# Kernel optimization log

Measured on AMD Instinct MI355X. Metric: run time of the kernel, lower is better.

Reference implementation:

```python
import jax, jax.numpy as jnp
import numpy as np

XZ = jnp.array([0, 2])
XY = jnp.array([0, 1])
YZ = jnp.array([1, 2])


def _bilinear(plane, uv):
    """plane: (C,R,R) as (C,H,W); uv: (N,2) in [0,1], uv[:,0]->width, uv[:,1]->height.
    Border padding + align_corners=True semantics (grid_sample style)."""
    R = plane.shape[-1]
    xy = jnp.clip(uv, 0.0, 1.0) * (R - 1)
    x, y = xy[:, 0], xy[:, 1]
    x0 = jnp.floor(x)
    y0 = jnp.floor(y)
    x0i = jnp.clip(x0.astype(jnp.int32), 0, R - 1)
    y0i = jnp.clip(y0.astype(jnp.int32), 0, R - 1)
    x1i = jnp.clip(x0i + 1, 0, R - 1)
    y1i = jnp.clip(y0i + 1, 0, R - 1)
    wx = (x - x0)[None, :]  # (1,N)
    wy = (y - y0)[None, :]
    f00 = plane[:, y0i, x0i]  # (C,N)
    f01 = plane[:, y0i, x1i]
    f10 = plane[:, y1i, x0i]
    f11 = plane[:, y1i, x1i]
    top = f00 * (1.0 - wx) + f01 * wx
    bot = f10 * (1.0 - wx) + f11 * wx
    return (top * (1.0 - wy) + bot * wy).T  # (N,C)


def _sample_triplane(p, c_xz, c_xy, c_yz):
    """p: (bs,N,3) in [0,1]; planes: (bs,C,R,R). Returns (bs,N,C) summed over planes."""
    def per_batch(pb, fxz, fxy, fyz):
        return (_bilinear(fxz, pb[:, XZ])
                + _bilinear(fxy, pb[:, XY])
                + _bilinear(fyz, pb[:, YZ]))
    return jax.vmap(per_batch)(p, c_xz, c_xy, c_yz)


def setup_inputs() -> dict:
    key = jax.random.key(0)
    ks = jax.random.split(key, 12)
    bs, ns, C, S, R = 2, 50000, 32, 8, 128
    inp = {
        "query_pos": jax.random.uniform(ks[0], (bs, ns, 3), dtype=jnp.float32),
        "c_xz": jax.random.normal(ks[1], (bs, C, R, R), dtype=jnp.float32),
        "c_xy": jax.random.normal(ks[2], (bs, C, R, R), dtype=jnp.float32),
        "c_yz": jax.random.normal(ks[3], (bs, C, R, R), dtype=jnp.float32),
        # offset weights scaled small so sampled points stay mostly in-bounds
        "W_off": jax.random.normal(ks[4], (C, S * 3), dtype=jnp.float32) * 0.01,
        "b_off": jnp.zeros((S * 3,), dtype=jnp.float32),
        "W_w": jax.random.normal(ks[5], (C, S), dtype=jnp.float32) * 0.1,
        "b_w": jnp.zeros((S,), dtype=jnp.float32),
        "W_v": jax.random.normal(ks[6], (C, C), dtype=jnp.float32) * (1.0 / np.sqrt(C)),
        "b_v": jnp.zeros((C,), dtype=jnp.float32),
        "W_out": jax.random.normal(ks[7], (C, C), dtype=jnp.float32) * (1.0 / np.sqrt(C)),
        "b_out": jnp.zeros((C,), dtype=jnp.float32),
    }
    return inp


def reference(query_pos, c_xz, c_xy, c_yz, W_off, b_off, W_w, b_w, W_v, b_v, W_out, b_out):
    bs, ns, _ = query_pos.shape
    S = W_w.shape[1]
    # round 1: sample tri-plane features at query points
    feature = _sample_triplane(query_pos, c_xz, c_xy, c_yz)  # (bs,ns,C)
    # predict per-query sample offsets and weights
    off = (feature @ W_off + b_off).reshape(bs, ns, S, 3)
    w = (feature @ W_w + b_w).reshape(bs, ns, S, 1)
    pts = off + query_pos[:, :, None, :]  # (bs,ns,S,3)
    # round 2: sample at deformed points
    aux = _sample_triplane(pts.reshape(bs, ns * S, 3), c_xz, c_xy, c_yz)
    v = aux.reshape(bs, ns, S, -1) @ W_v + b_v  # (bs,ns,S,C)
    out = (v * w).sum(-2)                        # weighted reduce over samples
    out = out @ W_out + b_out + feature          # residual
    return out  # (bs,ns,C)
```

## Files before the change

kernel.cpp:

```cpp
#include <hip/hip_runtime.h>
#include <hip/hip_fp16.h>

#define BS 2
#define NS 50000
#define CCH 32
#define RR 128
#define SS 8

typedef float v2f __attribute__((ext_vector_type(2)));


__device__ __forceinline__ v2f unpk(unsigned u) {
    __half2 h = __builtin_bit_cast(__half2, u);
    float2 f = __half22float2(h);
    v2f r; r.x = f.x; r.y = f.y;
    return r;
}

__global__ __launch_bounds__(256)
void prep(const float* __restrict__ cxz,
          const float* __restrict__ cxy,
          const float* __restrict__ cyz,
          const float* __restrict__ Wv, const float* __restrict__ bv,
          const float* __restrict__ Wout,
          unsigned short* __restrict__ tp, float* __restrict__ Wc,
          float* __restrict__ bvw) {
    __shared__ float lds[32 * 129];
    int tid = threadIdx.x;
    int row = blockIdx.x;
    if (row < BS * 3 * RR) {
        int y  = row & 127;
        int pl = (row >> 7) % 3;
        int b  = row / 384;
        const float* src = (pl == 0) ? cxz : ((pl == 1) ? cxy : cyz);
        const float* sp = src + (((size_t)(b * CCH)) << 14) + (y << 7);
#pragma unroll
        for (int i = 0; i < 16; ++i) {
            int c = (tid >> 7) + 2 * i;
            int x = tid & 127;
            lds[c * 129 + x] = sp[((size_t)c << 14) + x];
        }
        __syncthreads();
        ushort2* dst = (ushort2*)(tp + ((size_t)row << 12));
#pragma unroll
        for (int i = 0; i < 8; ++i) {
            int c2 = tid & 15;
            int x  = (tid >> 4) + 16 * i;
            ushort2 v;
            v.x = __half_as_ushort(__float2half(lds[(2 * c2) * 129 + x]));
            v.y = __half_as_ushort(__float2half(lds[(2 * c2 + 1) * 129 + x]));
            dst[(x << 4) + c2] = v;
        }
    } else {
        int t = (row - BS * 3 * RR) * 256 + tid;
        int c = t >> 5, j = t & 31;
        float acc = 0.f;
#pragma unroll
        for (int k = 0; k < 32; ++k) acc += Wv[c * 32 + k] * Wout[k * 32 + j];
        Wc[t] = acc;
        if (t < 32) {
            float a2 = 0.f;
#pragma unroll
            for (int k = 0; k < 32; ++k) a2 += bv[k] * Wout[k * 32 + t];
            bvw[t] = a2;
        }
    }
}

struct f4v { v2f lo, hi; };

__device__ __forceinline__ f4v sample3_h(const uint2* __restrict__ P0,
                                         float p0, float p1, float p2) {
    float ux[3] = {p0, p0, p1};
    float uy[3] = {p2, p1, p2};
    v2f rlo = {0.f, 0.f}, rhi = {0.f, 0.f};
#pragma unroll
    for (int pl = 0; pl < 3; ++pl) {
        float x = fminf(fmaxf(ux[pl], 0.f), 1.f) * 127.f;
        float y = fminf(fmaxf(uy[pl], 0.f), 1.f) * 127.f;
        float x0f = floorf(x), y0f = floorf(y);
        int x0 = (int)x0f, y0 = (int)y0f;
        int x1 = min(x0 + 1, 127), y1 = min(y0 + 1, 127);
        float wx = x - x0f, wy = y - y0f;
        const uint2* P = P0 + ((size_t)pl << 17);
        int r0 = (y0 << 10), r1 = (y1 << 10);
        uint2 u00 = P[r0 + (x0 << 3)];
        uint2 u01 = P[r0 + (x1 << 3)];
        uint2 u10 = P[r1 + (x0 << 3)];
        uint2 u11 = P[r1 + (x1 << 3)];
        v2f wx2 = {wx, wx}, wy2 = {wy, wy};
        {
            v2f f00 = unpk(u00.x), f01 = unpk(u01.x);
            v2f t = __builtin_elementwise_fma(wx2, f01 - f00, f00);
            v2f f10 = unpk(u10.x), f11 = unpk(u11.x);
            v2f bo = __builtin_elementwise_fma(wx2, f11 - f10, f10);
            rlo += __builtin_elementwise_fma(wy2, bo - t, t);
        }
        {
            v2f f00 = unpk(u00.y), f01 = unpk(u01.y);
            v2f t = __builtin_elementwise_fma(wx2, f01 - f00, f00);
            v2f f10 = unpk(u10.y), f11 = unpk(u11.y);
            v2f bo = __builtin_elementwise_fma(wx2, f11 - f10, f10);
            rhi += __builtin_elementwise_fma(wy2, bo - t, t);
        }
    }
    f4v r; r.lo = rlo; r.hi = rhi; return r;
}

#define GETE(v, idx) (((idx) & 2) ? (((idx) & 1) ? (v).hi.y : (v).hi.x) \
                                  : (((idx) & 1) ? (v).lo.y : (v).lo.x))
#define GETC(v, idx) __shfl(GETE(v, idx), base | ((idx) >> 2), 64)

__global__ __launch_bounds__(256)
void eda_main(const float* __restrict__ qp, const unsigned short* __restrict__ tp,
              const float* __restrict__ Woff, const float* __restrict__ boff,
              const float* __restrict__ Ww, const float* __restrict__ bw,
              const float* __restrict__ Wc, const float* __restrict__ bvw,
              const float* __restrict__ bout, float* __restrict__ out) {
    __shared__ v2f sWcat[32][8][2];
    __shared__ v2f sWc[32][8][2];
    __shared__ float sbcat[32];
    __shared__ float sbvw[32];
    __shared__ float sbout[32];

    int tid = threadIdx.x;
    for (int i = tid; i < 1024; i += 256) {
        int k = i >> 5, j = i & 31;
        ((float*)sWcat)[i] = (j < 24) ? Woff[k * 24 + j] : Ww[k * 8 + (j - 24)];
        ((float*)sWc)[i]   = Wc[i];
    }
    if (tid < 32) {
        sbcat[tid] = (tid < 24) ? boff[tid] : bw[tid - 24];
        sbvw[tid]  = bvw[tid];
        sbout[tid] = bout[tid];
    }
    __syncthreads();

    int lane = tid & 7;
    int base = tid & 56;
    int b  = blockIdx.x & 1;
    int qi = (blockIdx.x >> 1) * 32 + (tid >> 3);
    int qq = min(qi, NS - 1);

    const float* p = qp + ((size_t)b * NS + qq) * 3;
    float p0 = p[0], p1 = p[1], p2 = p[2];

    const uint2* P0 = (const uint2*)tp + (((size_t)(b * 3)) << 17) + lane;

    f4v feat = sample3_h(P0, p0, p1, p2);

    f4v cat;
    cat.lo.x = sbcat[(lane << 2) + 0]; cat.lo.y = sbcat[(lane << 2) + 1];
    cat.hi.x = sbcat[(lane << 2) + 2]; cat.hi.y = sbcat[(lane << 2) + 3];
#pragma unroll
    for (int k = 0; k < 32; ++k) {
        float fc = GETC(feat, k);
        v2f fc2 = {fc, fc};
        cat.lo = __builtin_elementwise_fma(fc2, sWcat[k][lane][0], cat.lo);
        cat.hi = __builtin_elementwise_fma(fc2, sWcat[k][lane][1], cat.hi);
    }

    float w_s[SS], o0[SS], o1[SS], o2[SS];
#pragma unroll
    for (int s = 0; s < SS; ++s) {
        w_s[s] = GETC(cat, 24 + s);
        o0[s]  = GETC(cat, 3 * s + 0);
        o1[s]  = GETC(cat, 3 * s + 1);
        o2[s]  = GETC(cat, 3 * s + 2);
    }

    f4v wa; wa.lo = (v2f){0.f, 0.f}; wa.hi = (v2f){0.f, 0.f};
    float wsum = 0.f;
#pragma unroll
    for (int s = 0; s < SS; ++s) {
        f4v aux = sample3_h(P0, p0 + o0[s], p1 + o1[s], p2 + o2[s]);
        v2f w2 = {w_s[s], w_s[s]};
        wa.lo = __builtin_elementwise_fma(w2, aux.lo, wa.lo);
        wa.hi = __builtin_elementwise_fma(w2, aux.hi, wa.hi);
        wsum += w_s[s];
    }

    v2f ws2 = {wsum, wsum};
    v2f blo = {sbout[(lane << 2) + 0], sbout[(lane << 2) + 1]};
    v2f bhi = {sbout[(lane << 2) + 2], sbout[(lane << 2) + 3]};
    v2f vlo = {sbvw[(lane << 2) + 0], sbvw[(lane << 2) + 1]};
    v2f vhi = {sbvw[(lane << 2) + 2], sbvw[(lane << 2) + 3]};
    v2f olo = __builtin_elementwise_fma(ws2, vlo, blo) + feat.lo;
    v2f ohi = __builtin_elementwise_fma(ws2, vhi, bhi) + feat.hi;
#pragma unroll
    for (int k = 0; k < 32; ++k) {
        float wc = GETC(wa, k);
        v2f wc2 = {wc, wc};
        olo = __builtin_elementwise_fma(wc2, sWc[k][lane][0], olo);
        ohi = __builtin_elementwise_fma(wc2, sWc[k][lane][1], ohi);
    }

    if (qi < NS) {
        float4 o4 = make_float4(olo.x, olo.y, ohi.x, ohi.y);
        *(float4*)(out + ((size_t)b * NS + qi) * 32 + (lane << 2)) = o4;
    }
}

extern "C" void kernel_launch(void* const* d_in, const int* in_sizes, int n_in,
                              void* d_out, int out_size, void* d_ws, size_t ws_size,
                              hipStream_t stream) {
    const float* qp   = (const float*)d_in[0];
    const float* cxz  = (const float*)d_in[1];
    const float* cxy  = (const float*)d_in[2];
    const float* cyz  = (const float*)d_in[3];
    const float* Woff = (const float*)d_in[4];
    const float* boff = (const float*)d_in[5];
    const float* Ww   = (const float*)d_in[6];
    const float* bw   = (const float*)d_in[7];
    const float* Wv   = (const float*)d_in[8];
    const float* bv   = (const float*)d_in[9];
    const float* Wout = (const float*)d_in[10];
    const float* bout = (const float*)d_in[11];
    float* out = (float*)d_out;

    unsigned short* tp = (unsigned short*)d_ws;
    float* Wc  = (float*)((char*)d_ws + (size_t)BS * 3 * RR * RR * CCH * 2);
    float* bvw = Wc + 1024;

    prep<<<BS * 3 * RR + 4, 256, 0, stream>>>(cxz, cxy, cyz, Wv, bv, Wout, tp, Wc, bvw);
    eda_main<<<2 * ((NS + 31) / 32), 256, 0, stream>>>(qp, tp, Woff, boff, Ww, bw,
                                                       Wc, bvw, bout, out);
}
```

Before: 141.5 us.

## Batch tap loads for two samples before evaluating, shrink blocks to 128 threads

Restructures trilinear sampling so all 12 gather loads for a sample are issued first, and two deformed samples' taps are loaded together before any arithmetic, increasing memory-level parallelism. Bilinear weights are precomputed as four corner weights, so each tap becomes a direct FMA. Block size drops to 128 threads with 16 queries per block, and the tail bounds checks are removed because NS divides evenly by 16. More live loads raise register pressure, which may reduce occupancy.

```diff
diff --git a/kernel.cpp b/kernel.cpp
--- a/kernel.cpp
+++ b/kernel.cpp
@@ -9,13 +9,6 @@
 
 typedef float v2f __attribute__((ext_vector_type(2)));
 
-
-__device__ __forceinline__ v2f unpk(unsigned u) {
-    __half2 h = __builtin_bit_cast(__half2, u);
-    float2 f = __half22float2(h);
-    v2f r; r.x = f.x; r.y = f.y;
-    return r;
-}
 
 __global__ __launch_bounds__(256)
 void prep(const float* __restrict__ cxz,
@@ -67,51 +60,60 @@
     }
 }
 
+
+struct Taps { uint2 u[12]; float wgt[12]; };
+
+__device__ __forceinline__ void load_plane(const uint2* __restrict__ P,
+                                           float px, float py,
+                                           uint2* u, float* wgt) {
+    float x = fminf(fmaxf(px, 0.f), 1.f) * 127.f;
+    float y = fminf(fmaxf(py, 0.f), 1.f) * 127.f;
+    float x0f = floorf(x), y0f = floorf(y);
+    int x0 = (int)x0f, y0 = (int)y0f;
+    int x1 = min(x0 + 1, 127), y1 = min(y0 + 1, 127);
+    float wx = x - x0f, wy = y - y0f;
+    int r0 = (y0 << 10), r1 = (y1 << 10);
+    u[0] = P[r0 + (x0 << 3)];
+    u[1] = P[r0 + (x1 << 3)];
+    u[2] = P[r1 + (x0 << 3)];
+    u[3] = P[r1 + (x1 << 3)];
+    float w11 = wx * wy;
+    wgt[1] = wx - w11;
+    wgt[2] = wy - w11;
+    wgt[0] = 1.f - wx - wgt[2];
+    wgt[3] = w11;
+}
+
+__device__ __forceinline__ Taps load_taps(const uint2* __restrict__ P0,
+                                          float p0, float p1, float p2) {
+    Taps t;
+    load_plane(P0,                      p0, p2, t.u + 0, t.wgt + 0);
+    load_plane(P0 + ((size_t)1 << 17),  p0, p1, t.u + 4, t.wgt + 4);
+    load_plane(P0 + ((size_t)2 << 17),  p1, p2, t.u + 8, t.wgt + 8);
+    return t;
+}
+
+__device__ __forceinline__ void acc4(v2f& lo, v2f& hi, uint2 u, float w) {
+    __half2 a = __builtin_bit_cast(__half2, u.x);
+    __half2 b = __builtin_bit_cast(__half2, u.y);
+    lo.x = fmaf(__half2float(a.x), w, lo.x);
+    lo.y = fmaf(__half2float(a.y), w, lo.y);
+    hi.x = fmaf(__half2float(b.x), w, hi.x);
+    hi.y = fmaf(__half2float(b.y), w, hi.y);
+}
+
+__device__ __forceinline__ void eval_taps(const Taps& t, v2f& lo, v2f& hi) {
+#pragma unroll
+    for (int i = 0; i < 12; ++i) acc4(lo, hi, t.u[i], t.wgt[i]);
+}
+
 struct f4v { v2f lo, hi; };
-
-__device__ __forceinline__ f4v sample3_h(const uint2* __restrict__ P0,
-                                         float p0, float p1, float p2) {
-    float ux[3] = {p0, p0, p1};
-    float uy[3] = {p2, p1, p2};
-    v2f rlo = {0.f, 0.f}, rhi = {0.f, 0.f};
-#pragma unroll
-    for (int pl = 0; pl < 3; ++pl) {
-        float x = fminf(fmaxf(ux[pl], 0.f), 1.f) * 127.f;
-        float y = fminf(fmaxf(uy[pl], 0.f), 1.f) * 127.f;
-        float x0f = floorf(x), y0f = floorf(y);
-        int x0 = (int)x0f, y0 = (int)y0f;
-        int x1 = min(x0 + 1, 127), y1 = min(y0 + 1, 127);
-        float wx = x - x0f, wy = y - y0f;
-        const uint2* P = P0 + ((size_t)pl << 17);
-        int r0 = (y0 << 10), r1 = (y1 << 10);
-        uint2 u00 = P[r0 + (x0 << 3)];
-        uint2 u01 = P[r0 + (x1 << 3)];
-        uint2 u10 = P[r1 + (x0 << 3)];
-        uint2 u11 = P[r1 + (x1 << 3)];
-        v2f wx2 = {wx, wx}, wy2 = {wy, wy};
-        {
-            v2f f00 = unpk(u00.x), f01 = unpk(u01.x);
-            v2f t = __builtin_elementwise_fma(wx2, f01 - f00, f00);
-            v2f f10 = unpk(u10.x), f11 = unpk(u11.x);
-            v2f bo = __builtin_elementwise_fma(wx2, f11 - f10, f10);
-            rlo += __builtin_elementwise_fma(wy2, bo - t, t);
-        }
-        {
-            v2f f00 = unpk(u00.y), f01 = unpk(u01.y);
-            v2f t = __builtin_elementwise_fma(wx2, f01 - f00, f00);
-            v2f f10 = unpk(u10.y), f11 = unpk(u11.y);
-            v2f bo = __builtin_elementwise_fma(wx2, f11 - f10, f10);
-            rhi += __builtin_elementwise_fma(wy2, bo - t, t);
-        }
-    }
-    f4v r; r.lo = rlo; r.hi = rhi; return r;
-}
 
 #define GETE(v, idx) (((idx) & 2) ? (((idx) & 1) ? (v).hi.y : (v).hi.x) \
                                   : (((idx) & 1) ? (v).lo.y : (v).lo.x))
 #define GETC(v, idx) __shfl(GETE(v, idx), base | ((idx) >> 2), 64)
 
-__global__ __launch_bounds__(256)
+__global__ __launch_bounds__(128)
 void eda_main(const float* __restrict__ qp, const unsigned short* __restrict__ tp,
               const float* __restrict__ Woff, const float* __restrict__ boff,
               const float* __restrict__ Ww, const float* __restrict__ bw,
@@ -124,7 +126,7 @@
     __shared__ float sbout[32];
 
     int tid = threadIdx.x;
-    for (int i = tid; i < 1024; i += 256) {
+    for (int i = tid; i < 1024; i += 128) {
         int k = i >> 5, j = i & 31;
         ((float*)sWcat)[i] = (j < 24) ? Woff[k * 24 + j] : Ww[k * 8 + (j - 24)];
         ((float*)sWc)[i]   = Wc[i];
@@ -139,15 +141,18 @@
     int lane = tid & 7;
     int base = tid & 56;
     int b  = blockIdx.x & 1;
-    int qi = (blockIdx.x >> 1) * 32 + (tid >> 3);
-    int qq = min(qi, NS - 1);
-
-    const float* p = qp + ((size_t)b * NS + qq) * 3;
+    int qi = (blockIdx.x >> 1) * 16 + (tid >> 3);
+
+    const float* p = qp + ((size_t)b * NS + qi) * 3;
     float p0 = p[0], p1 = p[1], p2 = p[2];
 
     const uint2* P0 = (const uint2*)tp + (((size_t)(b * 3)) << 17) + lane;
 
-    f4v feat = sample3_h(P0, p0, p1, p2);
+    f4v feat; feat.lo = (v2f){0.f, 0.f}; feat.hi = (v2f){0.f, 0.f};
+    {
+        Taps t = load_taps(P0, p0, p1, p2);
+        eval_taps(t, feat.lo, feat.hi);
+    }
 
     f4v cat;
     cat.lo.x = sbcat[(lane << 2) + 0]; cat.lo.y = sbcat[(lane << 2) + 1];
@@ -172,12 +177,20 @@
     f4v wa; wa.lo = (v2f){0.f, 0.f}; wa.hi = (v2f){0.f, 0.f};
     float wsum = 0.f;
 #pragma unroll
-    for (int s = 0; s < SS; ++s) {
-        f4v aux = sample3_h(P0, p0 + o0[s], p1 + o1[s], p2 + o2[s]);
-        v2f w2 = {w_s[s], w_s[s]};
-        wa.lo = __builtin_elementwise_fma(w2, aux.lo, wa.lo);
-        wa.hi = __builtin_elementwise_fma(w2, aux.hi, wa.hi);
-        wsum += w_s[s];
+    for (int s = 0; s < SS; s += 2) {
+        Taps t0 = load_taps(P0, p0 + o0[s],     p1 + o1[s],     p2 + o2[s]);
+        Taps t1 = load_taps(P0, p0 + o0[s + 1], p1 + o1[s + 1], p2 + o2[s + 1]);
+        f4v a0; a0.lo = (v2f){0.f, 0.f}; a0.hi = (v2f){0.f, 0.f};
+        f4v a1; a1.lo = (v2f){0.f, 0.f}; a1.hi = (v2f){0.f, 0.f};
+        eval_taps(t0, a0.lo, a0.hi);
+        eval_taps(t1, a1.lo, a1.hi);
+        v2f w20 = {w_s[s], w_s[s]};
+        v2f w21 = {w_s[s + 1], w_s[s + 1]};
+        wa.lo = __builtin_elementwise_fma(w20, a0.lo, wa.lo);
+        wa.hi = __builtin_elementwise_fma(w20, a0.hi, wa.hi);
+        wa.lo = __builtin_elementwise_fma(w21, a1.lo, wa.lo);
+        wa.hi = __builtin_elementwise_fma(w21, a1.hi, wa.hi);
+        wsum += w_s[s] + w_s[s + 1];
     }
 
     v2f ws2 = {wsum, wsum};
@@ -195,10 +208,8 @@
         ohi = __builtin_elementwise_fma(wc2, sWc[k][lane][1], ohi);
     }
 
-    if (qi < NS) {
-        float4 o4 = make_float4(olo.x, olo.y, ohi.x, ohi.y);
-        *(float4*)(out + ((size_t)b * NS + qi) * 32 + (lane << 2)) = o4;
-    }
+    float4 o4 = make_float4(olo.x, olo.y, ohi.x, ohi.y);
+    *(float4*)(out + ((size_t)b * NS + qi) * 32 + (lane << 2)) = o4;
 }
 
 extern "C" void kernel_launch(void* const* d_in, const int* in_sizes, int n_in,
@@ -223,6 +234,6 @@
     float* bvw = Wc + 1024;
 
     prep<<<BS * 3 * RR + 4, 256, 0, stream>>>(cxz, cxy, cyz, Wv, bv, Wout, tp, Wc, bvw);
-    eda_main<<<2 * ((NS + 31) / 32), 256, 0, stream>>>(qp, tp, Woff, boff, Ww, bw,
-                                                       Wc, bvw, bout, out);
-}
+    eda_main<<<2 * (NS / 16), 128, 0, stream>>>(qp, tp, Woff, boff, Ww, bw,
+                                                Wc, bvw, bout, out);
+}
```

After: 140.2 us. About the same (-0.9%).

## Use 4 lanes per query with 16-byte gathers and weight-form bilinear

Applied to the files above, without the earlier changes.

Each query is now handled by 4 lanes instead of 8, and each lane loads 8 fp16 channels as one uint4 rather than 4 channels as a uint2. Block size drops to 128 threads while still covering 32 queries per block. Bilinear interpolation is rewritten as four corner weights accumulated with scalar FMAs, replacing the lerp form. The aim is to halve the number of gather instructions and the redundant coordinate math per query. The cost is more registers per lane and fewer threads to hide gather latency.

```diff
diff --git a/kernel.cpp b/kernel.cpp
--- a/kernel.cpp
+++ b/kernel.cpp
@@ -9,13 +9,6 @@
 
 typedef float v2f __attribute__((ext_vector_type(2)));
 
-
-__device__ __forceinline__ v2f unpk(unsigned u) {
-    __half2 h = __builtin_bit_cast(__half2, u);
-    float2 f = __half22float2(h);
-    v2f r; r.x = f.x; r.y = f.y;
-    return r;
-}
 
 __global__ __launch_bounds__(256)
 void prep(const float* __restrict__ cxz,
@@ -67,64 +60,80 @@
     }
 }
 
-struct f4v { v2f lo, hi; };
-
-__device__ __forceinline__ f4v sample3_h(const uint2* __restrict__ P0,
-                                         float p0, float p1, float p2) {
-    float ux[3] = {p0, p0, p1};
-    float uy[3] = {p2, p1, p2};
-    v2f rlo = {0.f, 0.f}, rhi = {0.f, 0.f};
-#pragma unroll
-    for (int pl = 0; pl < 3; ++pl) {
-        float x = fminf(fmaxf(ux[pl], 0.f), 1.f) * 127.f;
-        float y = fminf(fmaxf(uy[pl], 0.f), 1.f) * 127.f;
-        float x0f = floorf(x), y0f = floorf(y);
-        int x0 = (int)x0f, y0 = (int)y0f;
-        int x1 = min(x0 + 1, 127), y1 = min(y0 + 1, 127);
-        float wx = x - x0f, wy = y - y0f;
-        const uint2* P = P0 + ((size_t)pl << 17);
-        int r0 = (y0 << 10), r1 = (y1 << 10);
-        uint2 u00 = P[r0 + (x0 << 3)];
-        uint2 u01 = P[r0 + (x1 << 3)];
-        uint2 u10 = P[r1 + (x0 << 3)];
-        uint2 u11 = P[r1 + (x1 << 3)];
-        v2f wx2 = {wx, wx}, wy2 = {wy, wy};
-        {
-            v2f f00 = unpk(u00.x), f01 = unpk(u01.x);
-            v2f t = __builtin_elementwise_fma(wx2, f01 - f00, f00);
-            v2f f10 = unpk(u10.x), f11 = unpk(u11.x);
-            v2f bo = __builtin_elementwise_fma(wx2, f11 - f10, f10);
-            rlo += __builtin_elementwise_fma(wy2, bo - t, t);
-        }
-        {
-            v2f f00 = unpk(u00.y), f01 = unpk(u01.y);
-            v2f t = __builtin_elementwise_fma(wx2, f01 - f00, f00);
-            v2f f10 = unpk(u10.y), f11 = unpk(u11.y);
-            v2f bo = __builtin_elementwise_fma(wx2, f11 - f10, f10);
-            rhi += __builtin_elementwise_fma(wy2, bo - t, t);
-        }
-    }
-    f4v r; r.lo = rlo; r.hi = rhi; return r;
-}
-
-#define GETE(v, idx) (((idx) & 2) ? (((idx) & 1) ? (v).hi.y : (v).hi.x) \
-                                  : (((idx) & 1) ? (v).lo.y : (v).lo.x))
-#define GETC(v, idx) __shfl(GETE(v, idx), base | ((idx) >> 2), 64)
-
-__global__ __launch_bounds__(256)
+
+struct f8 { v2f a[4]; };
+
+__device__ __forceinline__ void acc8(f8& acc, uint4 u, float w) {
+    __half2 h0 = __builtin_bit_cast(__half2, u.x);
+    __half2 h1 = __builtin_bit_cast(__half2, u.y);
+    __half2 h2 = __builtin_bit_cast(__half2, u.z);
+    __half2 h3 = __builtin_bit_cast(__half2, u.w);
+    acc.a[0].x = fmaf(__half2float(h0.x), w, acc.a[0].x);
+    acc.a[0].y = fmaf(__half2float(h0.y), w, acc.a[0].y);
+    acc.a[1].x = fmaf(__half2float(h1.x), w, acc.a[1].x);
+    acc.a[1].y = fmaf(__half2float(h1.y), w, acc.a[1].y);
+    acc.a[2].x = fmaf(__half2float(h2.x), w, acc.a[2].x);
+    acc.a[2].y = fmaf(__half2float(h2.y), w, acc.a[2].y);
+    acc.a[3].x = fmaf(__half2float(h3.x), w, acc.a[3].x);
+    acc.a[3].y = fmaf(__half2float(h3.y), w, acc.a[3].y);
+}
+
+__device__ __forceinline__ void axq(float p, int& i0, int& i1, float& w) {
+    float x = fminf(fmaxf(p, 0.f), 1.f) * 127.f;
+    float f = floorf(x);
+    i0 = (int)f;
+    i1 = min(i0 + 1, 127);
+    w = x - f;
+}
+
+__device__ __forceinline__ void plane_acc(f8& acc, const uint4* __restrict__ P,
+                                          int xi0, int xi1, float wx,
+                                          int yi0, int yi1, float wy) {
+    int r0 = yi0 << 9, r1 = yi1 << 9;
+    int c0 = xi0 << 2, c1 = xi1 << 2;
+    uint4 u00 = P[r0 + c0];
+    uint4 u01 = P[r0 + c1];
+    uint4 u10 = P[r1 + c0];
+    uint4 u11 = P[r1 + c1];
+    float w11 = wx * wy;
+    float w01 = wx - w11;
+    float w10 = wy - w11;
+    float w00 = 1.f - wx - w10;
+    acc8(acc, u00, w00);
+    acc8(acc, u01, w01);
+    acc8(acc, u10, w10);
+    acc8(acc, u11, w11);
+}
+
+__device__ __forceinline__ void sample3(f8& acc, const uint4* __restrict__ P0,
+                                        float p0, float p1, float p2) {
+    int a0i0, a0i1, a1i0, a1i1, a2i0, a2i1;
+    float w0, w1, w2;
+    axq(p0, a0i0, a0i1, w0);
+    axq(p1, a1i0, a1i1, w1);
+    axq(p2, a2i0, a2i1, w2);
+    plane_acc(acc, P0,             a0i0, a0i1, w0, a2i0, a2i1, w2);
+    plane_acc(acc, P0 + (1 << 16), a0i0, a0i1, w0, a1i0, a1i1, w1);
+    plane_acc(acc, P0 + (2 << 16), a1i0, a1i1, w1, a2i0, a2i1, w2);
+}
+
+#define GETE(v, idx) (((idx) & 1) ? (v).a[((idx) >> 1) & 3].y : (v).a[((idx) >> 1) & 3].x)
+#define GETC(v, idx) __shfl(GETE(v, idx), base | ((idx) >> 3), 64)
+
+__global__ __launch_bounds__(128)
 void eda_main(const float* __restrict__ qp, const unsigned short* __restrict__ tp,
               const float* __restrict__ Woff, const float* __restrict__ boff,
               const float* __restrict__ Ww, const float* __restrict__ bw,
               const float* __restrict__ Wc, const float* __restrict__ bvw,
               const float* __restrict__ bout, float* __restrict__ out) {
-    __shared__ v2f sWcat[32][8][2];
-    __shared__ v2f sWc[32][8][2];
+    __shared__ v2f sWcat[32][4][4];
+    __shared__ v2f sWc[32][4][4];
     __shared__ float sbcat[32];
     __shared__ float sbvw[32];
     __shared__ float sbout[32];
 
     int tid = threadIdx.x;
-    for (int i = tid; i < 1024; i += 256) {
+    for (int i = tid; i < 1024; i += 128) {
         int k = i >> 5, j = i & 31;
         ((float*)sWcat)[i] = (j < 24) ? Woff[k * 24 + j] : Ww[k * 8 + (j - 24)];
         ((float*)sWc)[i]   = Wc[i];
@@ -136,28 +145,33 @@
     }
     __syncthreads();
 
-    int lane = tid & 7;
-    int base = tid & 56;
+    int lane = tid & 3;
+    int base = tid & 60;
     int b  = blockIdx.x & 1;
-    int qi = (blockIdx.x >> 1) * 32 + (tid >> 3);
+    int qi = (blockIdx.x >> 1) * 32 + (tid >> 2);
     int qq = min(qi, NS - 1);
 
     const float* p = qp + ((size_t)b * NS + qq) * 3;
     float p0 = p[0], p1 = p[1], p2 = p[2];
 
-    const uint2* P0 = (const uint2*)tp + (((size_t)(b * 3)) << 17) + lane;
-
-    f4v feat = sample3_h(P0, p0, p1, p2);
-
-    f4v cat;
-    cat.lo.x = sbcat[(lane << 2) + 0]; cat.lo.y = sbcat[(lane << 2) + 1];
-    cat.hi.x = sbcat[(lane << 2) + 2]; cat.hi.y = sbcat[(lane << 2) + 3];
+    const uint4* P0 = (const uint4*)tp + (((size_t)(b * 3)) << 16) + lane;
+
+    f8 feat = {};
+    sample3(feat, P0, p0, p1, p2);
+
+    f8 cat;
+#pragma unroll
+    for (int e = 0; e < 4; ++e) {
+        cat.a[e].x = sbcat[(lane << 3) + 2 * e];
+        cat.a[e].y = sbcat[(lane << 3) + 2 * e + 1];
+    }
 #pragma unroll
     for (int k = 0; k < 32; ++k) {
         float fc = GETC(feat, k);
         v2f fc2 = {fc, fc};
-        cat.lo = __builtin_elementwise_fma(fc2, sWcat[k][lane][0], cat.lo);
-        cat.hi = __builtin_elementwise_fma(fc2, sWcat[k][lane][1], cat.hi);
+#pragma unroll
+        for (int e = 0; e < 4; ++e)
+            cat.a[e] = __builtin_elementwise_fma(fc2, sWcat[k][lane][e], cat.a[e]);
     }
 
     float w_s[SS], o0[SS], o1[SS], o2[SS];
@@ -169,35 +183,40 @@
         o2[s]  = GETC(cat, 3 * s + 2);
     }
 
-    f4v wa; wa.lo = (v2f){0.f, 0.f}; wa.hi = (v2f){0.f, 0.f};
+    f8 wa = {};
     float wsum = 0.f;
 #pragma unroll
     for (int s = 0; s < SS; ++s) {
-        f4v aux = sample3_h(P0, p0 + o0[s], p1 + o1[s], p2 + o2[s]);
+        f8 aux = {};
+        sample3(aux, P0, p0 + o0[s], p1 + o1[s], p2 + o2[s]);
         v2f w2 = {w_s[s], w_s[s]};
-        wa.lo = __builtin_elementwise_fma(w2, aux.lo, wa.lo);
-        wa.hi = __builtin_elementwise_fma(w2, aux.hi, wa.hi);
+#pragma unroll
+        for (int e = 0; e < 4; ++e)
+            wa.a[e] = __builtin_elementwise_fma(w2, aux.a[e], wa.a[e]);
         wsum += w_s[s];
     }
 
+    f8 o;
     v2f ws2 = {wsum, wsum};
-    v2f blo = {sbout[(lane << 2) + 0], sbout[(lane << 2) + 1]};
-    v2f bhi = {sbout[(lane << 2) + 2], sbout[(lane << 2) + 3]};
-    v2f vlo = {sbvw[(lane << 2) + 0], sbvw[(lane << 2) + 1]};
-    v2f vhi = {sbvw[(lane << 2) + 2], sbvw[(lane << 2) + 3]};
-    v2f olo = __builtin_elementwise_fma(ws2, vlo, blo) + feat.lo;
-    v2f ohi = __builtin_elementwise_fma(ws2, vhi, bhi) + feat.hi;
+#pragma unroll
+    for (int e = 0; e < 4; ++e) {
+        v2f bo  = {sbout[(lane << 3) + 2 * e], sbout[(lane << 3) + 2 * e + 1]};
+        v2f bv2 = {sbvw[(lane << 3) + 2 * e], sbvw[(lane << 3) + 2 * e + 1]};
+        o.a[e] = __builtin_elementwise_fma(ws2, bv2, bo) + feat.a[e];
+    }
 #pragma unroll
     for (int k = 0; k < 32; ++k) {
         float wc = GETC(wa, k);
         v2f wc2 = {wc, wc};
-        olo = __builtin_elementwise_fma(wc2, sWc[k][lane][0], olo);
-        ohi = __builtin_elementwise_fma(wc2, sWc[k][lane][1], ohi);
+#pragma unroll
+        for (int e = 0; e < 4; ++e)
+            o.a[e] = __builtin_elementwise_fma(wc2, sWc[k][lane][e], o.a[e]);
     }
 
     if (qi < NS) {
-        float4 o4 = make_float4(olo.x, olo.y, ohi.x, ohi.y);
-        *(float4*)(out + ((size_t)b * NS + qi) * 32 + (lane << 2)) = o4;
+        float* dst = out + ((size_t)b * NS + qi) * 32 + (lane << 3);
+        *(float4*)dst       = make_float4(o.a[0].x, o.a[0].y, o.a[1].x, o.a[1].y);
+        *(float4*)(dst + 4) = make_float4(o.a[2].x, o.a[2].y, o.a[3].x, o.a[3].y);
     }
 }
 
@@ -223,6 +242,7 @@
     float* bvw = Wc + 1024;
 
     prep<<<BS * 3 * RR + 4, 256, 0, stream>>>(cxz, cxy, cyz, Wv, bv, Wout, tp, Wc, bvw);
-    eda_main<<<2 * ((NS + 31) / 32), 256, 0, stream>>>(qp, tp, Woff, boff, Ww, bw,
+    int blocks_per_batch = (NS + 31) / 32;
+    eda_main<<<2 * blocks_per_batch, 128, 0, stream>>>(qp, tp, Woff, boff, Ww, bw,
                                                        Wc, bvw, bout, out);
 }
```

Measured after the change: 138.3 us. 1.02x faster.

## Pack horizontal texel pairs in triplane layout and software-pipeline sample loads

Applied to the files above, without the earlier changes.

The prep kernel now stores each fp16 texel together with its x+1 neighbour in one 32-bit word, so a bilinear tap needs two 16-byte row loads per plane instead of four 8-byte loads. The main kernel splits sampling into a load phase and an evaluate phase and prefetches the next offset sample's loads while evaluating the current one. It also issues the first feature loads before staging the weights in LDS so their latency is hidden. In exchange the packed table is twice as large, raising prep write traffic and cache footprint, and holding a second sample's loads in flight raises register pressure.

```diff
diff --git a/kernel.cpp b/kernel.cpp
--- a/kernel.cpp
+++ b/kernel.cpp
@@ -9,13 +9,6 @@
 
 typedef float v2f __attribute__((ext_vector_type(2)));
 
-
-__device__ __forceinline__ v2f unpk(unsigned u) {
-    __half2 h = __builtin_bit_cast(__half2, u);
-    float2 f = __half22float2(h);
-    v2f r; r.x = f.x; r.y = f.y;
-    return r;
-}
 
 __global__ __launch_bounds__(256)
 void prep(const float* __restrict__ cxz,
@@ -23,7 +16,7 @@
           const float* __restrict__ cyz,
           const float* __restrict__ Wv, const float* __restrict__ bv,
           const float* __restrict__ Wout,
-          unsigned short* __restrict__ tp, float* __restrict__ Wc,
+          unsigned* __restrict__ tp, float* __restrict__ Wc,
           float* __restrict__ bvw) {
     __shared__ float lds[32 * 129];
     int tid = threadIdx.x;
@@ -41,15 +34,16 @@
             lds[c * 129 + x] = sp[((size_t)c << 14) + x];
         }
         __syncthreads();
-        ushort2* dst = (ushort2*)(tp + ((size_t)row << 12));
-#pragma unroll
-        for (int i = 0; i < 8; ++i) {
-            int c2 = tid & 15;
-            int x  = (tid >> 4) + 16 * i;
-            ushort2 v;
-            v.x = __half_as_ushort(__float2half(lds[(2 * c2) * 129 + x]));
-            v.y = __half_as_ushort(__float2half(lds[(2 * c2 + 1) * 129 + x]));
-            dst[(x << 4) + c2] = v;
+        unsigned* dst = tp + ((size_t)row << 12);
+#pragma unroll
+        for (int i = 0; i < 16; ++i) {
+            int idx = tid + 256 * i;
+            int c = idx & 31;
+            int x = idx >> 5;
+            int x1 = min(x + 1, 127);
+            unsigned h0 = __half_as_ushort(__float2half(lds[c * 129 + x]));
+            unsigned h1 = __half_as_ushort(__float2half(lds[c * 129 + x1]));
+            dst[(x << 5) + c] = h0 | (h1 << 16);
         }
     } else {
         int t = (row - BS * 3 * RR) * 256 + tid;
@@ -67,44 +61,65 @@
     }
 }
 
-struct f4v { v2f lo, hi; };
-
-__device__ __forceinline__ f4v sample3_h(const uint2* __restrict__ P0,
-                                         float p0, float p1, float p2) {
-    float ux[3] = {p0, p0, p1};
-    float uy[3] = {p2, p1, p2};
-    v2f rlo = {0.f, 0.f}, rhi = {0.f, 0.f};
-#pragma unroll
-    for (int pl = 0; pl < 3; ++pl) {
-        float x = fminf(fmaxf(ux[pl], 0.f), 1.f) * 127.f;
-        float y = fminf(fmaxf(uy[pl], 0.f), 1.f) * 127.f;
-        float x0f = floorf(x), y0f = floorf(y);
-        int x0 = (int)x0f, y0 = (int)y0f;
-        int x1 = min(x0 + 1, 127), y1 = min(y0 + 1, 127);
-        float wx = x - x0f, wy = y - y0f;
-        const uint2* P = P0 + ((size_t)pl << 17);
-        int r0 = (y0 << 10), r1 = (y1 << 10);
-        uint2 u00 = P[r0 + (x0 << 3)];
-        uint2 u01 = P[r0 + (x1 << 3)];
-        uint2 u10 = P[r1 + (x0 << 3)];
-        uint2 u11 = P[r1 + (x1 << 3)];
-        v2f wx2 = {wx, wx}, wy2 = {wy, wy};
-        {
-            v2f f00 = unpk(u00.x), f01 = unpk(u01.x);
-            v2f t = __builtin_elementwise_fma(wx2, f01 - f00, f00);
-            v2f f10 = unpk(u10.x), f11 = unpk(u11.x);
-            v2f bo = __builtin_elementwise_fma(wx2, f11 - f10, f10);
-            rlo += __builtin_elementwise_fma(wy2, bo - t, t);
-        }
-        {
-            v2f f00 = unpk(u00.y), f01 = unpk(u01.y);
-            v2f t = __builtin_elementwise_fma(wx2, f01 - f00, f00);
-            v2f f10 = unpk(u10.y), f11 = unpk(u11.y);
-            v2f bo = __builtin_elementwise_fma(wx2, f11 - f10, f10);
-            rhi += __builtin_elementwise_fma(wy2, bo - t, t);
-        }
-    }
-    f4v r; r.lo = rlo; r.hi = rhi; return r;
+
+struct f4 { v2f lo, hi; };
+
+struct Samp { uint4 u[6]; float wc0, wc1, wr1, wr2; };
+
+__device__ __forceinline__ Samp load_samp(const uint4* __restrict__ P0,
+                                          float p0, float p1, float p2) {
+    Samp t;
+    float x0c = fminf(fmaxf(p0, 0.f), 1.f) * 127.f;
+    float x1c = fminf(fmaxf(p1, 0.f), 1.f) * 127.f;
+    float x2c = fminf(fmaxf(p2, 0.f), 1.f) * 127.f;
+    int i0 = min((int)x0c, 126);
+    t.wc0 = x0c - (float)i0;
+    int i1 = min((int)x1c, 126);
+    t.wc1 = x1c - (float)i1;
+    float f1 = floorf(x1c);
+    int r10 = (int)f1, r11 = min(r10 + 1, 127);
+    t.wr1 = x1c - f1;
+    float f2 = floorf(x2c);
+    int r20 = (int)f2, r21 = min(r20 + 1, 127);
+    t.wr2 = x2c - f2;
+
+    const uint4* Pxz = P0;
+    const uint4* Pxy = P0 + (1 << 17);
+    const uint4* Pyz = P0 + (2 << 17);
+    int c0 = i0 << 3, c1 = i1 << 3;
+    int R10 = r10 << 10, R11 = r11 << 10;
+    int R20 = r20 << 10, R21 = r21 << 10;
+    t.u[0] = Pxz[R20 + c0];  t.u[1] = Pxz[R21 + c0];
+    t.u[2] = Pxy[R10 + c0];  t.u[3] = Pxy[R11 + c0];
+    t.u[4] = Pyz[R20 + c1];  t.u[5] = Pyz[R21 + c1];
+    return t;
+}
+
+__device__ __forceinline__ void eval_row(f4& acc, uint4 u, float wA, float wB) {
+    __half2 h0 = __builtin_bit_cast(__half2, u.x);
+    __half2 h1 = __builtin_bit_cast(__half2, u.y);
+    __half2 h2 = __builtin_bit_cast(__half2, u.z);
+    __half2 h3 = __builtin_bit_cast(__half2, u.w);
+    acc.lo.x = fmaf(__half2float(h0.y), wB, fmaf(__half2float(h0.x), wA, acc.lo.x));
+    acc.lo.y = fmaf(__half2float(h1.y), wB, fmaf(__half2float(h1.x), wA, acc.lo.y));
+    acc.hi.x = fmaf(__half2float(h2.y), wB, fmaf(__half2float(h2.x), wA, acc.hi.x));
+    acc.hi.y = fmaf(__half2float(h3.y), wB, fmaf(__half2float(h3.x), wA, acc.hi.y));
+}
+
+__device__ __forceinline__ void eval_plane(f4& acc, uint4 ua, uint4 ub,
+                                           float wx, float wy) {
+    float wB1 = wx * wy;
+    float wB0 = wx - wB1;
+    float wA1 = wy - wB1;
+    float wA0 = 1.f - wx - wA1;
+    eval_row(acc, ua, wA0, wB0);
+    eval_row(acc, ub, wA1, wB1);
+}
+
+__device__ __forceinline__ void eval_samp(const Samp& t, f4& acc) {
+    eval_plane(acc, t.u[0], t.u[1], t.wc0, t.wr2);
+    eval_plane(acc, t.u[2], t.u[3], t.wc0, t.wr1);
+    eval_plane(acc, t.u[4], t.u[5], t.wc1, t.wr2);
 }
 
 #define GETE(v, idx) (((idx) & 2) ? (((idx) & 1) ? (v).hi.y : (v).hi.x) \
@@ -112,30 +127,18 @@
 #define GETC(v, idx) __shfl(GETE(v, idx), base | ((idx) >> 2), 64)
 
 __global__ __launch_bounds__(256)
-void eda_main(const float* __restrict__ qp, const unsigned short* __restrict__ tp,
+void eda_main(const float* __restrict__ qp, const unsigned* __restrict__ tp,
               const float* __restrict__ Woff, const float* __restrict__ boff,
               const float* __restrict__ Ww, const float* __restrict__ bw,
               const float* __restrict__ Wc, const float* __restrict__ bvw,
               const float* __restrict__ bout, float* __restrict__ out) {
-    __shared__ v2f sWcat[32][8][2];
-    __shared__ v2f sWc[32][8][2];
+    __shared__ float sWcat[32][32];
+    __shared__ float sWc2[32][32];
     __shared__ float sbcat[32];
     __shared__ float sbvw[32];
     __shared__ float sbout[32];
 
     int tid = threadIdx.x;
-    for (int i = tid; i < 1024; i += 256) {
-        int k = i >> 5, j = i & 31;
-        ((float*)sWcat)[i] = (j < 24) ? Woff[k * 24 + j] : Ww[k * 8 + (j - 24)];
-        ((float*)sWc)[i]   = Wc[i];
-    }
-    if (tid < 32) {
-        sbcat[tid] = (tid < 24) ? boff[tid] : bw[tid - 24];
-        sbvw[tid]  = bvw[tid];
-        sbout[tid] = bout[tid];
-    }
-    __syncthreads();
-
     int lane = tid & 7;
     int base = tid & 56;
     int b  = blockIdx.x & 1;
@@ -145,59 +148,82 @@
     const float* p = qp + ((size_t)b * NS + qq) * 3;
     float p0 = p[0], p1 = p[1], p2 = p[2];
 
-    const uint2* P0 = (const uint2*)tp + (((size_t)(b * 3)) << 17) + lane;
-
-    f4v feat = sample3_h(P0, p0, p1, p2);
-
-    f4v cat;
+    const uint4* P0 = (const uint4*)tp + (((size_t)(b * 3)) << 17) + lane;
+
+    Samp fs = load_samp(P0, p0, p1, p2);
+
+    for (int i = tid; i < 1024; i += 256) {
+        int k = i >> 5, j = i & 31;
+        ((float*)sWcat)[i] = (j < 24) ? Woff[k * 24 + j] : Ww[k * 8 + (j - 24)];
+        ((float*)sWc2)[i]  = Wc[i];
+    }
+    if (tid < 32) {
+        sbcat[tid] = (tid < 24) ? boff[tid] : bw[tid - 24];
+        sbvw[tid]  = bvw[tid];
+        sbout[tid] = bout[tid];
+    }
+    __syncthreads();
+
+    f4 feat; feat.lo = (v2f){0.f, 0.f}; feat.hi = (v2f){0.f, 0.f};
+    eval_samp(fs, feat);
+
+    f4 cat;
     cat.lo.x = sbcat[(lane << 2) + 0]; cat.lo.y = sbcat[(lane << 2) + 1];
     cat.hi.x = sbcat[(lane << 2) + 2]; cat.hi.y = sbcat[(lane << 2) + 3];
 #pragma unroll
     for (int k = 0; k < 32; ++k) {
         float fc = GETC(feat, k);
+        const v2f* wp = (const v2f*)&sWcat[k][lane << 2];
         v2f fc2 = {fc, fc};
-        cat.lo = __builtin_elementwise_fma(fc2, sWcat[k][lane][0], cat.lo);
-        cat.hi = __builtin_elementwise_fma(fc2, sWcat[k][lane][1], cat.hi);
-    }
-
-    float w_s[SS], o0[SS], o1[SS], o2[SS];
+        cat.lo = __builtin_elementwise_fma(fc2, wp[0], cat.lo);
+        cat.hi = __builtin_elementwise_fma(fc2, wp[1], cat.hi);
+    }
+
+    f4 wa; wa.lo = (v2f){0.f, 0.f}; wa.hi = (v2f){0.f, 0.f};
+    float wsum = 0.f;
+    float w_cur = GETC(cat, 24);
+    Samp cur = load_samp(P0, p0 + GETC(cat, 0), p1 + GETC(cat, 1), p2 + GETC(cat, 2));
+    Samp nxt;
+    float w_nxt;
 #pragma unroll
     for (int s = 0; s < SS; ++s) {
-        w_s[s] = GETC(cat, 24 + s);
-        o0[s]  = GETC(cat, 3 * s + 0);
-        o1[s]  = GETC(cat, 3 * s + 1);
-        o2[s]  = GETC(cat, 3 * s + 2);
-    }
-
-    f4v wa; wa.lo = (v2f){0.f, 0.f}; wa.hi = (v2f){0.f, 0.f};
-    float wsum = 0.f;
-#pragma unroll
-    for (int s = 0; s < SS; ++s) {
-        f4v aux = sample3_h(P0, p0 + o0[s], p1 + o1[s], p2 + o2[s]);
-        v2f w2 = {w_s[s], w_s[s]};
+        if (s < SS - 1) {
+            w_nxt = GETC(cat, 24 + (s + 1));
+            nxt = load_samp(P0, p0 + GETC(cat, 3 * (s + 1) + 0),
+                                p1 + GETC(cat, 3 * (s + 1) + 1),
+                                p2 + GETC(cat, 3 * (s + 1) + 2));
+        }
+        f4 aux; aux.lo = (v2f){0.f, 0.f}; aux.hi = (v2f){0.f, 0.f};
+        eval_samp(cur, aux);
+        v2f w2 = {w_cur, w_cur};
         wa.lo = __builtin_elementwise_fma(w2, aux.lo, wa.lo);
         wa.hi = __builtin_elementwise_fma(w2, aux.hi, wa.hi);
-        wsum += w_s[s];
-    }
-
+        wsum += w_cur;
+        if (s < SS - 1) { cur = nxt; w_cur = w_nxt; }
+    }
+
+    f4 o;
     v2f ws2 = {wsum, wsum};
-    v2f blo = {sbout[(lane << 2) + 0], sbout[(lane << 2) + 1]};
-    v2f bhi = {sbout[(lane << 2) + 2], sbout[(lane << 2) + 3]};
-    v2f vlo = {sbvw[(lane << 2) + 0], sbvw[(lane << 2) + 1]};
-    v2f vhi = {sbvw[(lane << 2) + 2], sbvw[(lane << 2) + 3]};
-    v2f olo = __builtin_elementwise_fma(ws2, vlo, blo) + feat.lo;
-    v2f ohi = __builtin_elementwise_fma(ws2, vhi, bhi) + feat.hi;
+    {
+        v2f bo  = {sbout[(lane << 2) + 0], sbout[(lane << 2) + 1]};
+        v2f bv2 = {sbvw[(lane << 2) + 0], sbvw[(lane << 2) + 1]};
+        o.lo = __builtin_elementwise_fma(ws2, bv2, bo) + feat.lo;
+        v2f bo2 = {sbout[(lane << 2) + 2], sbout[(lane << 2) + 3]};
+        v2f bv3 = {sbvw[(lane << 2) + 2], sbvw[(lane << 2) + 3]};
+        o.hi = __builtin_elementwise_fma(ws2, bv3, bo2) + feat.hi;
+    }
 #pragma unroll
     for (int k = 0; k < 32; ++k) {
         float wc = GETC(wa, k);
+        const v2f* wp = (const v2f*)&sWc2[k][lane << 2];
         v2f wc2 = {wc, wc};
-        olo = __builtin_elementwise_fma(wc2, sWc[k][lane][0], olo);
-        ohi = __builtin_elementwise_fma(wc2, sWc[k][lane][1], ohi);
+        o.lo = __builtin_elementwise_fma(wc2, wp[0], o.lo);
+        o.hi = __builtin_elementwise_fma(wc2, wp[1], o.hi);
     }
 
     if (qi < NS) {
-        float4 o4 = make_float4(olo.x, olo.y, ohi.x, ohi.y);
-        *(float4*)(out + ((size_t)b * NS + qi) * 32 + (lane << 2)) = o4;
+        float* dst = out + ((size_t)b * NS + qi) * 32 + (lane << 2);
+        *(float4*)dst = make_float4(o.lo.x, o.lo.y, o.hi.x, o.hi.y);
     }
 }
 
@@ -218,11 +244,12 @@
     const float* bout = (const float*)d_in[11];
     float* out = (float*)d_out;
 
-    unsigned short* tp = (unsigned short*)d_ws;
-    float* Wc  = (float*)((char*)d_ws + (size_t)BS * 3 * RR * RR * CCH * 2);
+    unsigned* tp = (unsigned*)d_ws;
+    float* Wc  = (float*)((char*)d_ws + (size_t)BS * 3 * RR * RR * CCH * 4);
     float* bvw = Wc + 1024;
 
     prep<<<BS * 3 * RR + 4, 256, 0, stream>>>(cxz, cxy, cyz, Wv, bv, Wout, tp, Wc, bvw);
-    eda_main<<<2 * ((NS + 31) / 32), 256, 0, stream>>>(qp, tp, Woff, boff, Ww, bw,
+    int blocks_per_batch = (NS + 31) / 32;
+    eda_main<<<2 * blocks_per_batch, 256, 0, stream>>>(qp, tp, Woff, boff, Ww, bw,
                                                        Wc, bvw, bout, out);
 }
```

After: 135.9 us. -4.0%, faster.
